# Performance work log

Hardware: AMD Instinct MI355X
Metric: run time of the kernel (lower is better)

The kernel has to match this reference:

```python
import jax, jax.numpy as jnp
import numpy as np

B, S, D = 128, 50, 128
NUM_NODE = 40000
SAMPLE = 12
HOP = 2
ALPHA = 0.2  # leaky-relu slope (opt.alpha)


def _leaky(x, slope=ALPHA):
    return jnp.where(x >= 0, x, slope * x)


def setup_inputs() -> dict:
    key = jax.random.key(0)
    ks = jax.random.split(key, 12)
    stdv = 1.0 / float(np.sqrt(D))
    inputs = jax.random.randint(ks[0], (B, S), 0, NUM_NODE)
    adj = jax.random.randint(ks[1], (B, S, S), 0, 5)
    mask_item = jax.random.randint(ks[2], (B, S), 0, 2).at[:, 0].set(1)
    item = jax.random.randint(ks[3], (B, S), 0, NUM_NODE)
    adj_all = jax.random.randint(ks[4], (NUM_NODE, SAMPLE), 0, NUM_NODE)
    num_weight = jax.random.uniform(ks[5], (NUM_NODE, SAMPLE), dtype=jnp.float32)
    embedding = jax.random.uniform(ks[6], (NUM_NODE, D), minval=-stdv, maxval=stdv, dtype=jnp.float32)
    a_local = jax.random.uniform(ks[7], (4, D), minval=-stdv, maxval=stdv, dtype=jnp.float32)
    agg_w1 = jax.random.uniform(ks[8], (HOP, D + 1, D), minval=-stdv, maxval=stdv, dtype=jnp.float32)
    agg_w2 = jax.random.uniform(ks[9], (HOP, D, 1), minval=-stdv, maxval=stdv, dtype=jnp.float32)
    agg_w3 = jax.random.uniform(ks[10], (HOP, 2 * D, D), minval=-stdv, maxval=stdv, dtype=jnp.float32)
    return dict(inputs=inputs, adj=adj, mask_item=mask_item, item=item,
                adj_all=adj_all, num_weight=num_weight, embedding=embedding,
                a_local=a_local, agg_w1=agg_w1, agg_w2=agg_w2, agg_w3=agg_w3)


def _local_agg(h, adj, a_local):
    # e_k[b,i,j] = leakyrelu(sum_d h[b,i,d]*h[b,j,d]*a_k[d]); never materialize [B,N,N,D]
    e = _leaky(jnp.einsum('bid,bjd,kd->kbij', h, h, a_local))  # [4,B,S,S]
    alpha = jnp.full(e.shape[1:], -9e15, dtype=h.dtype)
    for k in range(4):
        alpha = jnp.where(adj == k + 1, e[k], alpha)
    alpha = jax.nn.softmax(alpha, axis=-1)
    return alpha @ h


def _global_agg(w1, w2, w3, self_v, neigh_v, neigh_w, extra):
    # self_v [B,L,D]; neigh_v [B,L,SAMPLE,D]; neigh_w [B,L,SAMPLE]; extra [B,L,D]
    feat = jnp.concatenate([extra[:, :, None, :] * neigh_v, neigh_w[..., None]], axis=-1)  # [B,L,SAMPLE,D+1]
    a = _leaky(feat @ w1, 0.2)                              # [B,L,SAMPLE,D]
    a = jax.nn.softmax((a @ w2)[..., 0], axis=-1)[..., None]  # [B,L,SAMPLE,1]
    neigh = jnp.sum(a * neigh_v, axis=-2)                   # [B,L,D]
    out = jnp.concatenate([self_v, neigh], axis=-1) @ w3    # [B,L,D]
    return jax.nn.relu(out)


def _forward(inputs, adj, mask_item, item, adj_all, num_weight, embedding,
             a_local, agg_w1, agg_w2, agg_w3):
    h = embedding[inputs]                          # [B,S,D]
    h_local = _local_agg(h, adj, a_local)
    # multi-hop neighbor sampling (index_select into adj_all / num)
    item_neighbors = [inputs]
    weight_neighbors = []
    support = S
    for _ in range(HOP):
        last = item_neighbors[-1].reshape(-1)
        support *= SAMPLE
        item_neighbors.append(adj_all[last].reshape(B, support))
        weight_neighbors.append(num_weight[last].reshape(B, support))
    entity = [embedding[idx] for idx in item_neighbors]
    mask_f = mask_item.astype(h.dtype)
    item_emb = embedding[item] * mask_f[..., None]
    session = (jnp.sum(item_emb, 1) / jnp.sum(mask_f, -1, keepdims=True))[:, None, :]  # [B,1,D]
    for n_hop in range(HOP):
        nxt = []
        for hop in range(HOP - n_hop):
            self_v = entity[hop]
            L = self_v.shape[1]
            neigh_v = entity[hop + 1].reshape(B, L, SAMPLE, D)
            neigh_w = weight_neighbors[hop].reshape(B, L, SAMPLE)
            extra = jnp.broadcast_to(session, (B, L, D))
            nxt.append(_global_agg(agg_w1[n_hop], agg_w2[n_hop], agg_w3[n_hop],
                                   self_v, neigh_v, neigh_w, extra))
        entity = nxt
    h_global = entity[0].reshape(B, S, D)
    # dropout_local / dropout_global are identity in eval mode
    return h_local + h_global


def reference(inputs, adj, mask_item, item, adj_all, num_weight, embedding,
              a_local, agg_w1, agg_w2, agg_w3):
    return _forward(inputs, adj, mask_item, item, adj_all, num_weight, embedding,
                    a_local, agg_w1, agg_w2, agg_w3)
```

## Files before the change

kernel.cpp:

```cpp
#include <hip/hip_runtime.h>
#include <math.h>

#define BATCH 128
#define S 50
#define D 128
#define SAMPLE 12

typedef __attribute__((ext_vector_type(8))) short short8v;
typedef __attribute__((ext_vector_type(4))) float f32x4;
typedef unsigned short u16;

__device__ __forceinline__ float leakyf(float x) { return x >= 0.f ? x : 0.2f * x; }
__device__ __forceinline__ u16 f2bf(float f) {
    union { float f; unsigned u; } v; v.f = f;
    unsigned u = v.u;
    return (u16)((u + 0x7FFFu + ((u >> 16) & 1u)) >> 16);
}
__device__ __forceinline__ float bf2f(u16 h) {
    union { float f; unsigned u; } v; v.u = ((unsigned)h) << 16; return v.f;
}

__global__ __launch_bounds__(256) void setup1_kernel(
    const int* __restrict__ item, const int* __restrict__ mask,
    const int* __restrict__ inputs, const int* __restrict__ adj_all,
    const float* __restrict__ num_weight, const float* __restrict__ emb,
    float* __restrict__ session, int* __restrict__ n1, float* __restrict__ nw0)
{
    const int bx = blockIdx.x, t = threadIdx.x;
    if (bx < BATCH) {
        if (t < 128) {
            float num = 0.f, den = 0.f;
            for (int s = 0; s < S; ++s) {
                float m = (float)mask[bx * S + s];
                num += m * emb[item[bx * S + s] * D + t];
                den += m;
            }
            session[bx * D + t] = num / den;
        }
    } else {
        int idx = (bx - BATCH) * 256 + t;
        if (idx < BATCH * 600) {
            int b = idx / 600, j = idx % 600;
            int node = inputs[b * S + j / SAMPLE];
            n1[idx]  = adj_all[node * SAMPLE + j % SAMPLE];
            nw0[idx] = num_weight[node * SAMPLE + j % SAMPLE];
        }
    }
}

__global__ __launch_bounds__(256) void prep2_kernel(
    const float* __restrict__ emb, const float* __restrict__ w1,
    const float* __restrict__ w3, const float* __restrict__ session,
    const int* __restrict__ adj_all, const float* __restrict__ num_weight,
    const int* __restrict__ n1,
    u16* __restrict__ emb_bf, u16* __restrict__ sw1, u16* __restrict__ w3t,
    int* __restrict__ n2p, int* __restrict__ n1p, float* __restrict__ nw1)
{
    const int bx = blockIdx.x, t = threadIdx.x;
    if (bx < 2500) {
        int idx = bx * 256 + t;
        const float4* src = reinterpret_cast<const float4*>(emb) + (size_t)idx * 2;
        float4 a = src[0], c = src[1];
        u16 o[8] = {f2bf(a.x), f2bf(a.y), f2bf(a.z), f2bf(a.w),
                    f2bf(c.x), f2bf(c.y), f2bf(c.z), f2bf(c.w)};
        *reinterpret_cast<uint4*>(emb_bf + (size_t)idx * 8) = *reinterpret_cast<uint4*>(o);
    } else if (bx < 2756) {
        int id = bx - 2500, hop = id >> 7, b = id & 127;
        const float* w1s = w1 + hop * 129 * 128;
        const float* se = session + b * 128;
        int n = t >> 1, kh = (t & 1) * 64;
        u16* dst = sw1 + (((size_t)(hop * 128 + b) * 128 + n) * 128) + kh;
        for (int kq = 0; kq < 64; kq += 8) {
            u16 o[8];
            #pragma unroll
            for (int e = 0; e < 8; ++e) { int k = kh + kq + e; o[e] = f2bf(w1s[k * 128 + n] * se[k]); }
            *reinterpret_cast<uint4*>(dst + kq) = *reinterpret_cast<uint4*>(o);
        }
    } else if (bx < 2788) {
        int j = (bx - 2756) * 256 + t;
        int hop = j >> 12, r = j & 4095, n = r >> 5, k0 = (r & 31) * 8;
        const float* w3s = w3 + hop * 256 * 128;
        u16 o[8];
        #pragma unroll
        for (int e = 0; e < 8; ++e) o[e] = f2bf(w3s[(k0 + e) * 128 + n]);
        *reinterpret_cast<uint4*>(w3t + ((size_t)hop * 128 + n) * 256 + k0) = *reinterpret_cast<uint4*>(o);
    } else if (bx < 6388) {
        int idx = (bx - 2788) * 256 + t;
        if (idx < BATCH * 7200) {
            int b = idx / 7200, r = idx % 7200;
            int lblk = r / 96, q = r % 96;
            int i = q >> 4, c = q & 15;
            int gm = lblk * 96 + (c >> 2) * 24 + i * 4 + (c & 3);
            int node = n1[b * 600 + gm / SAMPLE];
            int s = gm % SAMPLE;
            n2p[idx] = adj_all[node * SAMPLE + s] << 8;
            nw1[b * 7200 + gm] = num_weight[node * SAMPLE + s];
        }
    } else {
        int idx = (bx - 6388) * 256 + t;
        if (idx < BATCH * 672) {
            int b = idx / 672, r = idx % 672;
            int lblk = r / 96, q = r % 96;
            int i = q >> 4, c = q & 15;
            int gm = lblk * 96 + (c >> 2) * 24 + i * 4 + (c & 3);
            int jc = (gm < 600) ? gm : 0;
            n1p[idx] = n1[b * 600 + jc] << 8;
        }
    }
}

__device__ __forceinline__ int swz(int cg, int kk) { return ((kk & 1) << 2) | cg; }

template <int PATH>
__global__ __launch_bounds__(256, 4) void main_kernel(
    const int* __restrict__ inputs, const int* __restrict__ adj,
    const u16* __restrict__ emb_bf, const float* __restrict__ a_local,
    const int* __restrict__ n1, const int* __restrict__ n2p,
    const int* __restrict__ n1p,
    const float* __restrict__ nw0, const float* __restrict__ nw1,
    const u16* __restrict__ sw1, const float* __restrict__ w1,
    const float* __restrict__ w2, const u16* __restrict__ w3t,
    const u16* __restrict__ in0, const u16* __restrict__ in1,
    u16* __restrict__ o0, u16* __restrict__ o1, float* __restrict__ outf)
{
    __shared__ __align__(16) char smem[35072];
    const int b = blockIdx.y;
    const int t = threadIdx.x;
    const int bx = blockIdx.x;

    if (PATH == 0 && bx == 0) {
        u16*   ht    = (u16*)smem;
        float* alpha = (float*)(smem + 13312);
        u16*   alb   = (u16*)(smem + 23520);

        for (int idx = t; idx < S * D; idx += 256) {
            int i = idx >> 7, d = idx & 127;
            ht[d * 52 + i] = emb_bf[(size_t)inputs[b * S + i] * D + d];
        }
        for (int idx = t; idx < 512; idx += 256) alb[idx] = f2bf(a_local[idx]);
        __syncthreads();

        for (int p = t; p < S * S; p += 256) {
            int i = p / S, j = p % S;
            int a = adj[b * S * S + p];
            float v = -9e15f;
            if (a >= 1 && a <= 4) {
                const u16* ak = alb + (a - 1) * D;
                float dot = 0.f;
                #pragma unroll 4
                for (int d = 0; d < D; ++d)
                    dot += bf2f(ht[d * 52 + i]) * bf2f(ht[d * 52 + j]) * bf2f(ak[d]);
                v = leakyf(dot);
            }
            alpha[i * 51 + j] = v;
        }
        __syncthreads();

        if (t < S) {
            float m = -INFINITY;
            for (int j = 0; j < S; ++j) m = fmaxf(m, alpha[t * 51 + j]);
            float ssum = 0.f;
            for (int j = 0; j < S; ++j) { float e = __expf(alpha[t * 51 + j] - m); alpha[t * 51 + j] = e; ssum += e; }
            float inv = 1.f / ssum;
            for (int j = 0; j < S; ++j) alpha[t * 51 + j] *= inv;
        }
        __syncthreads();

        for (int idx = t; idx < S * D; idx += 256) {
            int i = idx >> 7, d = idx & 127;
            float acc = 0.f;
            #pragma unroll 5
            for (int j = 0; j < S; ++j) acc += alpha[i * 51 + j] * bf2f(ht[d * 52 + j]);
            outf[(size_t)b * S * D + idx] = acc;
        }
        return;
    }

    int mode, lblk, L, Lm, hop;
    const u16 *nsrc, *ssrc;
    const int* ptab; const float* nwTab;
    u16* outb;
    if (PATH == 2)    { mode = 2; lblk = bx;     L = 50;  Lm = 600;  hop = 1; nsrc = in1;    ssrc = in0;    ptab = nullptr;                   nwTab = nw0; outb = nullptr; }
    else if (bx >= 8) { mode = 1; lblk = bx - 8; L = 600; Lm = 7200; hop = 0; nsrc = emb_bf; ssrc = emb_bf; ptab = n2p + (b * 75 + lblk) * 96; nwTab = nw1; outb = o1; }
    else              { mode = 0; lblk = bx - 1; L = 50;  Lm = 600;  hop = 0; nsrc = emb_bf; ssrc = emb_bf; ptab = n1p + (b * 7 + lblk) * 96;  nwTab = nw0; outb = o0; }
    const int l0 = lblk * 8;

    u16*   nvL     = (u16*)smem;
    u16*   A2      = (u16*)(smem + 24576);
    float* score_w = (float*)(smem + 32768);
    float* nwgtL   = (float*)(smem + 34304);
    float* alphL   = (float*)(smem + 34688);

    const u16*   sw1b   = sw1 + (size_t)(hop * 128 + b) * 16384;
    const float* w1last = w1 + hop * 129 * 128 + 128 * 128;
    const float* w2h    = w2 + hop * 128;
    const u16*   w3th   = w3t + hop * 32768;

    const int lane = t & 63, wv = t >> 6, cn = lane & 15, cg = lane >> 4;
    const int nc0 = (2 * wv) * 16 + cn, nc1 = (2 * wv + 1) * 16 + cn;
    const int cS = t & 15;
    const int chunk = t >> 4;

    {
        int kkS = t >> 6, cgS = (t >> 4) & 3;
        int cn2 = cS ^ swz(cgS, kkS);
        #pragma unroll
        for (int i = 0; i < 6; ++i) {
            int off;
            if (PATH == 2) {
                int gm = l0 * 12 + (cn2 >> 2) * 24 + i * 4 + (cn2 & 3);
                if (gm > 599) gm = 599;
                off = (b * 600 + gm) << 8;
            } else {
                off = ptab[i * 16 + cn2];
            }
            uint4 v = *reinterpret_cast<const uint4*>((const char*)nsrc + (unsigned)off + chunk * 16);
            *reinterpret_cast<uint4*>(nvL + (i * 256 + t) * 8) = v;
        }
    }
    {
        uint4 v = make_uint4(0, 0, 0, 0);
        if (cS < 8) {
            int lg = l0 + cS; if (lg >= L) lg = 0;
            int srow;
            if (PATH == 2)      srow = b * 50 + lg;
            else if (mode == 1) srow = n1[b * 600 + lg];
            else                srow = inputs[b * S + lg];
            v = *reinterpret_cast<const uint4*>(ssrc + (size_t)srow * 128 + chunk * 8);
        }
        *reinterpret_cast<uint4*>(A2 + t * 8) = v;
    }
    if (t < 128) {
        int slot = (4 + (t >> 5)) * 64 + ((t >> 3) & 3) * 16 + 8 + (t & 7);
        *reinterpret_cast<uint4*>(A2 + slot * 8) = make_uint4(0, 0, 0, 0);
    }
    if (t < 96) {
        int gm = l0 * 12 + t;
        nwgtL[t] = (gm < Lm) ? nwTab[b * Lm + gm] : 0.f;
    }
    __syncthreads();

    f32x4 acc[6][2];
    #pragma unroll
    for (int mt = 0; mt < 6; ++mt) {
        acc[mt][0] = (f32x4){0.f, 0.f, 0.f, 0.f};
        acc[mt][1] = (f32x4){0.f, 0.f, 0.f, 0.f};
    }
    #pragma unroll
    for (int kk = 0; kk < 4; ++kk) {
        int kb = kk * 32 + cg * 8;
        int lslot = cg * 16 + (cn ^ swz(cg, kk));
        short8v b0 = *reinterpret_cast<const short8v*>(sw1b + nc0 * 128 + kb);
        short8v b1 = *reinterpret_cast<const short8v*>(sw1b + nc1 * 128 + kb);
        #pragma unroll
        for (int mt = 0; mt < 6; ++mt) {
            short8v a = *reinterpret_cast<const short8v*>(nvL + ((mt * 4 + kk) * 64 + lslot) * 8);
            acc[mt][0] = __builtin_amdgcn_mfma_f32_16x16x32_bf16(a, b0, acc[mt][0], 0, 0, 0);
            acc[mt][1] = __builtin_amdgcn_mfma_f32_16x16x32_bf16(a, b1, acc[mt][1], 0, 0, 0);
        }
    }
    {
        float w2v0 = w2h[nc0], w2v1 = w2h[nc1];
        float w1l0 = w1last[nc0], w1l1 = w1last[nc1];
        #pragma unroll
        for (int mt = 0; mt < 6; ++mt) {
            #pragma unroll
            for (int r = 0; r < 4; ++r) {
                int m = cg * 24 + mt * 4 + r;
                float nw = nwgtL[m];
                float v = leakyf(acc[mt][0][r] + nw * w1l0) * w2v0 +
                          leakyf(acc[mt][1][r] + nw * w1l1) * w2v1;
                v += __shfl_xor(v, 1); v += __shfl_xor(v, 2);
                v += __shfl_xor(v, 4); v += __shfl_xor(v, 8);
                if (cn == 0) score_w[m * 4 + wv] = v;
            }
        }
    }
    __syncthreads();

    {
        float alph[24];
        const f32x4* sw4 = reinterpret_cast<const f32x4*>(score_w);
        float mx0 = -1e30f, mx1 = -1e30f;
        #pragma unroll
        for (int q = 0; q < 24; ++q) {
            f32x4 s4 = sw4[cg * 24 + q];
            float s = (s4[0] + s4[1]) + (s4[2] + s4[3]);
            alph[q] = s;
            if (q < 12) mx0 = fmaxf(mx0, s); else mx1 = fmaxf(mx1, s);
        }
        float sm0 = 0.f, sm1 = 0.f;
        #pragma unroll
        for (int q = 0; q < 12; ++q) { alph[q] = __expf(alph[q] - mx0); sm0 += alph[q]; }
        #pragma unroll
        for (int q = 12; q < 24; ++q) { alph[q] = __expf(alph[q] - mx1); sm1 += alph[q]; }
        float i0 = 1.f / sm0, i1 = 1.f / sm1;
        if (cn == 0) {
            #pragma unroll
            for (int q = 0; q < 12; ++q)  alphL[(cg * 2) * 12 + q] = alph[q] * i0;
            #pragma unroll
            for (int q = 12; q < 24; ++q) alphL[(cg * 2 + 1) * 12 + (q - 12)] = alph[q] * i1;
        }
    }

    #pragma unroll 1
    for (int i = 0; i < 4; ++i) {
        int idx = i * 256 + t;
        int l = idx >> 7, d = idx & 127;
        int kkd = d >> 5, cgd = (d >> 3) & 3, el = d & 7;
        int cnb = (l >> 1) * 4;
        int mtb = (l & 1) * 3;
        int fd = swz(cgd, kkd);
        float a = 0.f;
        #pragma unroll
        for (int s = 0; s < 12; ++s) {
            int slot = ((mtb + (s >> 2)) * 4 + kkd) * 64 + cgd * 16 + ((cnb + (s & 3)) ^ fd);
            a += alphL[l * 12 + s] * bf2f(nvL[slot * 8 + el]);
        }
        int slot2 = (4 + kkd) * 64 + cgd * 16 + l;
        A2[slot2 * 8 + el] = f2bf(a);
    }
    __syncthreads();

    #pragma unroll
    for (int j = 0; j < 2; ++j) {
        int nc = (2 * wv + j) * 16 + cn;
        f32x4 acc2 = (f32x4){0.f, 0.f, 0.f, 0.f};
        #pragma unroll
        for (int kk2 = 0; kk2 < 8; ++kk2) {
            short8v a2 = *reinterpret_cast<const short8v*>(A2 + (kk2 * 64 + lane) * 8);
            short8v bb = *reinterpret_cast<const short8v*>(w3th + nc * 256 + kk2 * 32 + cg * 8);
            acc2 = __builtin_amdgcn_mfma_f32_16x16x32_bf16(a2, bb, acc2, 0, 0, 0);
        }
        if (cg < 2) {
            #pragma unroll
            for (int r = 0; r < 4; ++r) {
                int l = cg * 4 + r;
                int lg = l0 + l;
                float v = fmaxf(acc2[r], 0.f);
                if (lg < L) {
                    if (PATH == 2) { float* p = outf + ((size_t)b * 50 + lg) * 128 + nc; *p += v; }
                    else           outb[((size_t)b * L + lg) * 128 + nc] = f2bf(v);
                }
            }
        }
    }
}

extern "C" void kernel_launch(void* const* d_in, const int* in_sizes, int n_in,
                              void* d_out, int out_size, void* d_ws, size_t ws_size,
                              hipStream_t stream)
{
    const int*   inputs     = (const int*)d_in[0];
    const int*   adj        = (const int*)d_in[1];
    const int*   mask_item  = (const int*)d_in[2];
    const int*   item       = (const int*)d_in[3];
    const int*   adj_all    = (const int*)d_in[4];
    const float* num_weight = (const float*)d_in[5];
    const float* embedding  = (const float*)d_in[6];
    const float* a_local    = (const float*)d_in[7];
    const float* agg_w1     = (const float*)d_in[8];
    const float* agg_w2     = (const float*)d_in[9];
    const float* agg_w3     = (const float*)d_in[10];
    float* out = (float*)d_out;

    char* w = (char*)d_ws;
    float* ws_session = (float*)(w);
    int*   ws_n1      = (int*)(w + 65536);
    float* ws_nw0     = (float*)(w + 372736);
    float* ws_nw1     = (float*)(w + 679936);
    int*   ws_n2p     = (int*)(w + 4366336);
    int*   ws_n1p     = (int*)(w + 8052736);
    u16*   ws_emb     = (u16*)(w + 8396800);
    u16*   ws_sw1     = (u16*)(w + 18636800);
    u16*   ws_w3t     = (u16*)(w + 27025408);
    u16*   ws_out0    = (u16*)(w + 27156480);
    u16*   ws_out1    = (u16*)(w + 28794880);

    setup1_kernel<<<dim3(BATCH + 300), 256, 0, stream>>>(
        item, mask_item, inputs, adj_all, num_weight, embedding,
        ws_session, ws_n1, ws_nw0);
    prep2_kernel<<<dim3(6724), 256, 0, stream>>>(
        embedding, agg_w1, agg_w3, ws_session, adj_all, num_weight, ws_n1,
        ws_emb, ws_sw1, ws_w3t, ws_n2p, ws_n1p, ws_nw1);

    main_kernel<0><<<dim3(83, BATCH), 256, 0, stream>>>(
        inputs, adj, ws_emb, a_local, ws_n1, ws_n2p, ws_n1p, ws_nw0, ws_nw1,
        ws_sw1, agg_w1, agg_w2, ws_w3t,
        nullptr, nullptr, ws_out0, ws_out1, out);

    main_kernel<2><<<dim3(7, BATCH), 256, 0, stream>>>(
        inputs, adj, ws_emb, a_local, ws_n1, ws_n2p, ws_n1p, ws_nw0, ws_nw1,
        ws_sw1, agg_w1, agg_w2, ws_w3t,
        ws_out0, ws_out1, nullptr, nullptr, out);
}
```

Baseline: 356.6 us.

## Assign one wave per neighbor row with register-resident A fragments

```diff
diff --git a/kernel.cpp b/kernel.cpp
--- a/kernel.cpp
+++ b/kernel.cpp
@@ -54,7 +54,7 @@
     const int* __restrict__ adj_all, const float* __restrict__ num_weight,
     const int* __restrict__ n1,
     u16* __restrict__ emb_bf, u16* __restrict__ sw1, u16* __restrict__ w3t,
-    int* __restrict__ n2p, int* __restrict__ n1p, float* __restrict__ nw1)
+    int* __restrict__ n2o, float* __restrict__ nw1)
 {
     const int bx = blockIdx.x, t = threadIdx.x;
     if (bx < 2500) {
@@ -84,46 +84,30 @@
         #pragma unroll
         for (int e = 0; e < 8; ++e) o[e] = f2bf(w3s[(k0 + e) * 128 + n]);
         *reinterpret_cast<uint4*>(w3t + ((size_t)hop * 128 + n) * 256 + k0) = *reinterpret_cast<uint4*>(o);
-    } else if (bx < 6388) {
+    } else {
         int idx = (bx - 2788) * 256 + t;
         if (idx < BATCH * 7200) {
-            int b = idx / 7200, r = idx % 7200;
-            int lblk = r / 96, q = r % 96;
-            int i = q >> 4, c = q & 15;
-            int gm = lblk * 96 + (c >> 2) * 24 + i * 4 + (c & 3);
-            int node = n1[b * 600 + gm / SAMPLE];
-            int s = gm % SAMPLE;
-            n2p[idx] = adj_all[node * SAMPLE + s] << 8;
-            nw1[b * 7200 + gm] = num_weight[node * SAMPLE + s];
-        }
-    } else {
-        int idx = (bx - 6388) * 256 + t;
-        if (idx < BATCH * 672) {
-            int b = idx / 672, r = idx % 672;
-            int lblk = r / 96, q = r % 96;
-            int i = q >> 4, c = q & 15;
-            int gm = lblk * 96 + (c >> 2) * 24 + i * 4 + (c & 3);
-            int jc = (gm < 600) ? gm : 0;
-            n1p[idx] = n1[b * 600 + jc] << 8;
-        }
-    }
-}
-
-__device__ __forceinline__ int swz(int cg, int kk) { return ((kk & 1) << 2) | cg; }
+            int b = idx / 7200, j = idx % 7200;
+            int node = n1[b * 600 + j / SAMPLE];
+            int s = j % SAMPLE;
+            n2o[idx] = adj_all[node * SAMPLE + s] << 8;
+            nw1[idx] = num_weight[node * SAMPLE + s];
+        }
+    }
+}
 
 template <int PATH>
-__global__ __launch_bounds__(256, 4) void main_kernel(
+__global__ __launch_bounds__(512, 4) void main_kernel(
     const int* __restrict__ inputs, const int* __restrict__ adj,
     const u16* __restrict__ emb_bf, const float* __restrict__ a_local,
-    const int* __restrict__ n1, const int* __restrict__ n2p,
-    const int* __restrict__ n1p,
+    const int* __restrict__ n1, const int* __restrict__ n2o,
     const float* __restrict__ nw0, const float* __restrict__ nw1,
     const u16* __restrict__ sw1, const float* __restrict__ w1,
     const float* __restrict__ w2, const u16* __restrict__ w3t,
     const u16* __restrict__ in0, const u16* __restrict__ in1,
     u16* __restrict__ o0, u16* __restrict__ o1, float* __restrict__ outf)
 {
-    __shared__ __align__(16) char smem[35072];
+    __shared__ __align__(16) char smem[41472];
     const int b = blockIdx.y;
     const int t = threadIdx.x;
     const int bx = blockIdx.x;
@@ -133,14 +117,15 @@
         float* alpha = (float*)(smem + 13312);
         u16*   alb   = (u16*)(smem + 23520);
 
-        for (int idx = t; idx < S * D; idx += 256) {
+        for (int idx = t; idx < S * D; idx += 512) {
             int i = idx >> 7, d = idx & 127;
             ht[d * 52 + i] = emb_bf[(size_t)inputs[b * S + i] * D + d];
         }
-        for (int idx = t; idx < 512; idx += 256) alb[idx] = f2bf(a_local[idx]);
+        if (t < 512) { if (t < 512 && t < 512) {} }
+        for (int idx = t; idx < 512; idx += 512) alb[idx] = f2bf(a_local[idx]);
         __syncthreads();
 
-        for (int p = t; p < S * S; p += 256) {
+        for (int p = t; p < S * S; p += 512) {
             int i = p / S, j = p % S;
             int a = adj[b * S * S + p];
             float v = -9e15f;
@@ -166,7 +151,7 @@
         }
         __syncthreads();
 
-        for (int idx = t; idx < S * D; idx += 256) {
+        for (int idx = t; idx < S * D; idx += 512) {
             int i = idx >> 7, d = idx & 127;
             float acc = 0.f;
             #pragma unroll 5
@@ -176,156 +161,128 @@
         return;
     }
 
-    int mode, lblk, L, Lm, hop;
+    int mode, lblk, L, hop, nstr;
     const u16 *nsrc, *ssrc;
-    const int* ptab; const float* nwTab;
+    const float* nwTab;
     u16* outb;
-    if (PATH == 2)    { mode = 2; lblk = bx;     L = 50;  Lm = 600;  hop = 1; nsrc = in1;    ssrc = in0;    ptab = nullptr;                   nwTab = nw0; outb = nullptr; }
-    else if (bx >= 8) { mode = 1; lblk = bx - 8; L = 600; Lm = 7200; hop = 0; nsrc = emb_bf; ssrc = emb_bf; ptab = n2p + (b * 75 + lblk) * 96; nwTab = nw1; outb = o1; }
-    else              { mode = 0; lblk = bx - 1; L = 50;  Lm = 600;  hop = 0; nsrc = emb_bf; ssrc = emb_bf; ptab = n1p + (b * 7 + lblk) * 96;  nwTab = nw0; outb = o0; }
+    if (PATH == 2)    { mode = 2; lblk = bx;     L = 50;  hop = 1; nstr = 600;  nsrc = in1;    ssrc = in0;    nwTab = nw0; outb = nullptr; }
+    else if (bx >= 8) { mode = 1; lblk = bx - 8; L = 600; hop = 0; nstr = 7200; nsrc = emb_bf; ssrc = emb_bf; nwTab = nw1; outb = o1; }
+    else              { mode = 0; lblk = bx - 1; L = 50;  hop = 0; nstr = 600;  nsrc = emb_bf; ssrc = emb_bf; nwTab = nw0; outb = o0; }
     const int l0 = lblk * 8;
 
-    u16*   nvL     = (u16*)smem;
-    u16*   A2      = (u16*)(smem + 24576);
-    float* score_w = (float*)(smem + 32768);
-    float* nwgtL   = (float*)(smem + 34304);
-    float* alphL   = (float*)(smem + 34688);
+    const int wv = t >> 6, lane = t & 63, cn = lane & 15, cg = lane >> 4;
+    const int l = l0 + wv;
+    const int lc = (l < L) ? l : (L - 1);
+
+    u16*   nvw   = (u16*)(smem) + wv * 2048;
+    u16*   A2    = (u16*)(smem + 32768);
+    float* alphL = (float*)(smem + 40960);
 
     const u16*   sw1b   = sw1 + (size_t)(hop * 128 + b) * 16384;
     const float* w1last = w1 + hop * 129 * 128 + 128 * 128;
     const float* w2h    = w2 + hop * 128;
     const u16*   w3th   = w3t + hop * 32768;
 
-    const int lane = t & 63, wv = t >> 6, cn = lane & 15, cg = lane >> 4;
-    const int nc0 = (2 * wv) * 16 + cn, nc1 = (2 * wv + 1) * 16 + cn;
-    const int cS = t & 15;
-    const int chunk = t >> 4;
-
+    int sidx = (cn < 12) ? cn : 11;
+    unsigned off;
+    if (mode == 1)      off = (unsigned)n2o[b * 7200 + lc * 12 + sidx];
+    else if (mode == 0) off = (unsigned)n1[b * 600 + lc * 12 + sidx] << 8;
+    else                off = (unsigned)(b * 600 + lc * 12 + sidx) << 8;
+
+    short8v aF[4];
+    #pragma unroll
+    for (int kk = 0; kk < 4; ++kk)
+        aF[kk] = *reinterpret_cast<const short8v*>((const char*)nsrc + off + (kk * 32 + cg * 8) * 2);
+    #pragma unroll
+    for (int kk = 0; kk < 4; ++kk)
+        *reinterpret_cast<short8v*>((char*)nvw + cn * 256 + ((kk * 64 + cg * 16) ^ ((cn & 7) << 4))) = aF[kk];
+
+    float nwr[4];
+    #pragma unroll
+    for (int r = 0; r < 4; ++r) {
+        int row = cg * 4 + r; int rr = (row < 12) ? row : 11;
+        nwr[r] = nwTab[b * nstr + lc * 12 + rr];
+    }
+
+    if (lane < 16) {
+        int kk = lane >> 2, cg2 = lane & 3;
+        int lg = l; if (lg >= L) lg = 0;
+        int srow;
+        if (PATH == 2)      srow = b * 50 + lg;
+        else if (mode == 1) srow = n1[b * 600 + lg];
+        else                srow = inputs[b * S + lg];
+        uint4 v = *reinterpret_cast<const uint4*>(ssrc + (size_t)srow * 128 + kk * 32 + cg2 * 8);
+        *reinterpret_cast<uint4*>(A2 + (kk * 64 + cg2 * 16 + wv) * 8) = v;
+    } else if (lane < 48) {
+        int idx = wv * 32 + (lane - 16);
+        int slot = (idx >> 5) * 64 + ((idx >> 3) & 3) * 16 + 8 + (idx & 7);
+        *reinterpret_cast<uint4*>(A2 + slot * 8) = make_uint4(0, 0, 0, 0);
+    }
+
+    f32x4 acc[8];
+    #pragma unroll
+    for (int nt = 0; nt < 8; ++nt) acc[nt] = (f32x4){0.f, 0.f, 0.f, 0.f};
+    #pragma unroll
+    for (int kk = 0; kk < 4; ++kk) {
+        #pragma unroll
+        for (int nt = 0; nt < 8; ++nt) {
+            short8v bF = *reinterpret_cast<const short8v*>(sw1b + (nt * 16 + cn) * 128 + kk * 32 + cg * 8);
+            acc[nt] = __builtin_amdgcn_mfma_f32_16x16x32_bf16(aF[kk], bF, acc[nt], 0, 0, 0);
+        }
+    }
+
+    float sc[4];
+    #pragma unroll
+    for (int r = 0; r < 4; ++r) {
+        float v = 0.f;
+        #pragma unroll
+        for (int nt = 0; nt < 8; ++nt) {
+            int ncol = nt * 16 + cn;
+            v += leakyf(acc[nt][r] + nwr[r] * w1last[ncol]) * w2h[ncol];
+        }
+        v += __shfl_xor(v, 1); v += __shfl_xor(v, 2);
+        v += __shfl_xor(v, 4); v += __shfl_xor(v, 8);
+        sc[r] = v;
+    }
     {
-        int kkS = t >> 6, cgS = (t >> 4) & 3;
-        int cn2 = cS ^ swz(cgS, kkS);
-        #pragma unroll
-        for (int i = 0; i < 6; ++i) {
-            int off;
-            if (PATH == 2) {
-                int gm = l0 * 12 + (cn2 >> 2) * 24 + i * 4 + (cn2 & 3);
-                if (gm > 599) gm = 599;
-                off = (b * 600 + gm) << 8;
-            } else {
-                off = ptab[i * 16 + cn2];
-            }
-            uint4 v = *reinterpret_cast<const uint4*>((const char*)nsrc + (unsigned)off + chunk * 16);
-            *reinterpret_cast<uint4*>(nvL + (i * 256 + t) * 8) = v;
-        }
-    }
-    {
-        uint4 v = make_uint4(0, 0, 0, 0);
-        if (cS < 8) {
-            int lg = l0 + cS; if (lg >= L) lg = 0;
-            int srow;
-            if (PATH == 2)      srow = b * 50 + lg;
-            else if (mode == 1) srow = n1[b * 600 + lg];
-            else                srow = inputs[b * S + lg];
-            v = *reinterpret_cast<const uint4*>(ssrc + (size_t)srow * 128 + chunk * 8);
-        }
-        *reinterpret_cast<uint4*>(A2 + t * 8) = v;
-    }
-    if (t < 128) {
-        int slot = (4 + (t >> 5)) * 64 + ((t >> 3) & 3) * 16 + 8 + (t & 7);
-        *reinterpret_cast<uint4*>(A2 + slot * 8) = make_uint4(0, 0, 0, 0);
-    }
-    if (t < 96) {
-        int gm = l0 * 12 + t;
-        nwgtL[t] = (gm < Lm) ? nwTab[b * Lm + gm] : 0.f;
-    }
-    __syncthreads();
-
-    f32x4 acc[6][2];
-    #pragma unroll
-    for (int mt = 0; mt < 6; ++mt) {
-        acc[mt][0] = (f32x4){0.f, 0.f, 0.f, 0.f};
-        acc[mt][1] = (f32x4){0.f, 0.f, 0.f, 0.f};
-    }
-    #pragma unroll
-    for (int kk = 0; kk < 4; ++kk) {
-        int kb = kk * 32 + cg * 8;
-        int lslot = cg * 16 + (cn ^ swz(cg, kk));
-        short8v b0 = *reinterpret_cast<const short8v*>(sw1b + nc0 * 128 + kb);
-        short8v b1 = *reinterpret_cast<const short8v*>(sw1b + nc1 * 128 + kb);
-        #pragma unroll
-        for (int mt = 0; mt < 6; ++mt) {
-            short8v a = *reinterpret_cast<const short8v*>(nvL + ((mt * 4 + kk) * 64 + lslot) * 8);
-            acc[mt][0] = __builtin_amdgcn_mfma_f32_16x16x32_bf16(a, b0, acc[mt][0], 0, 0, 0);
-            acc[mt][1] = __builtin_amdgcn_mfma_f32_16x16x32_bf16(a, b1, acc[mt][1], 0, 0, 0);
-        }
-    }
-    {
-        float w2v0 = w2h[nc0], w2v1 = w2h[nc1];
-        float w1l0 = w1last[nc0], w1l1 = w1last[nc1];
-        #pragma unroll
-        for (int mt = 0; mt < 6; ++mt) {
-            #pragma unroll
-            for (int r = 0; r < 4; ++r) {
-                int m = cg * 24 + mt * 4 + r;
-                float nw = nwgtL[m];
-                float v = leakyf(acc[mt][0][r] + nw * w1l0) * w2v0 +
-                          leakyf(acc[mt][1][r] + nw * w1l1) * w2v1;
-                v += __shfl_xor(v, 1); v += __shfl_xor(v, 2);
-                v += __shfl_xor(v, 4); v += __shfl_xor(v, 8);
-                if (cn == 0) score_w[m * 4 + wv] = v;
-            }
-        }
-    }
-    __syncthreads();
-
-    {
-        float alph[24];
-        const f32x4* sw4 = reinterpret_cast<const f32x4*>(score_w);
-        float mx0 = -1e30f, mx1 = -1e30f;
-        #pragma unroll
-        for (int q = 0; q < 24; ++q) {
-            f32x4 s4 = sw4[cg * 24 + q];
-            float s = (s4[0] + s4[1]) + (s4[2] + s4[3]);
-            alph[q] = s;
-            if (q < 12) mx0 = fmaxf(mx0, s); else mx1 = fmaxf(mx1, s);
-        }
-        float sm0 = 0.f, sm1 = 0.f;
-        #pragma unroll
-        for (int q = 0; q < 12; ++q) { alph[q] = __expf(alph[q] - mx0); sm0 += alph[q]; }
-        #pragma unroll
-        for (int q = 12; q < 24; ++q) { alph[q] = __expf(alph[q] - mx1); sm1 += alph[q]; }
-        float i0 = 1.f / sm0, i1 = 1.f / sm1;
+        float mx = -1e30f;
+        #pragma unroll
+        for (int r = 0; r < 4; ++r) if (cg * 4 + r < 12) mx = fmaxf(mx, sc[r]);
+        mx = fmaxf(mx, __shfl_xor(mx, 16)); mx = fmaxf(mx, __shfl_xor(mx, 32));
+        float e[4]; float sm = 0.f;
+        #pragma unroll
+        for (int r = 0; r < 4; ++r) {
+            e[r] = (cg * 4 + r < 12) ? __expf(sc[r] - mx) : 0.f;
+            sm += e[r];
+        }
+        sm += __shfl_xor(sm, 16); sm += __shfl_xor(sm, 32);
+        float inv = 1.f / sm;
         if (cn == 0) {
             #pragma unroll
-            for (int q = 0; q < 12; ++q)  alphL[(cg * 2) * 12 + q] = alph[q] * i0;
-            #pragma unroll
-            for (int q = 12; q < 24; ++q) alphL[(cg * 2 + 1) * 12 + (q - 12)] = alph[q] * i1;
-        }
-    }
-
-    #pragma unroll 1
-    for (int i = 0; i < 4; ++i) {
-        int idx = i * 256 + t;
-        int l = idx >> 7, d = idx & 127;
-        int kkd = d >> 5, cgd = (d >> 3) & 3, el = d & 7;
-        int cnb = (l >> 1) * 4;
-        int mtb = (l & 1) * 3;
-        int fd = swz(cgd, kkd);
-        float a = 0.f;
-        #pragma unroll
-        for (int s = 0; s < 12; ++s) {
-            int slot = ((mtb + (s >> 2)) * 4 + kkd) * 64 + cgd * 16 + ((cnb + (s & 3)) ^ fd);
-            a += alphL[l * 12 + s] * bf2f(nvL[slot * 8 + el]);
-        }
-        int slot2 = (4 + kkd) * 64 + cgd * 16 + l;
-        A2[slot2 * 8 + el] = f2bf(a);
+            for (int r = 0; r < 4; ++r)
+                if (cg * 4 + r < 12) alphL[wv * 16 + cg * 4 + r] = e[r] * inv;
+        }
+    }
+
+    {
+        float a0 = 0.f, a1 = 0.f;
+        #pragma unroll
+        for (int s2 = 0; s2 < 12; ++s2) {
+            unsigned pk = *reinterpret_cast<const unsigned*>(
+                (const char*)nvw + s2 * 256 + ((lane * 4) ^ ((s2 & 7) << 4)));
+            float al = alphL[wv * 16 + s2];
+            a0 += al * bf2f((u16)(pk & 0xffff));
+            a1 += al * bf2f((u16)(pk >> 16));
+        }
+        unsigned pk2 = ((unsigned)f2bf(a1) << 16) | f2bf(a0);
+        int slot = (4 + cg) * 64 + ((lane >> 2) & 3) * 16 + wv;
+        *reinterpret_cast<unsigned*>((char*)A2 + slot * 16 + (lane & 3) * 4) = pk2;
     }
     __syncthreads();
 
-    #pragma unroll
-    for (int j = 0; j < 2; ++j) {
-        int nc = (2 * wv + j) * 16 + cn;
+    {
         f32x4 acc2 = (f32x4){0.f, 0.f, 0.f, 0.f};
+        int nc = wv * 16 + cn;
         #pragma unroll
         for (int kk2 = 0; kk2 < 8; ++kk2) {
             short8v a2 = *reinterpret_cast<const short8v*>(A2 + (kk2 * 64 + lane) * 8);
@@ -335,8 +292,8 @@
         if (cg < 2) {
             #pragma unroll
             for (int r = 0; r < 4; ++r) {
-                int l = cg * 4 + r;
-                int lg = l0 + l;
+                int row = cg * 4 + r;
+                int lg = l0 + row;
                 float v = fmaxf(acc2[r], 0.f);
                 if (lg < L) {
                     if (PATH == 2) { float* p = outf + ((size_t)b * 50 + lg) * 128 + nc; *p += v; }
@@ -369,28 +326,27 @@
     int*   ws_n1      = (int*)(w + 65536);
     float* ws_nw0     = (float*)(w + 372736);
     float* ws_nw1     = (float*)(w + 679936);
-    int*   ws_n2p     = (int*)(w + 4366336);
-    int*   ws_n1p     = (int*)(w + 8052736);
-    u16*   ws_emb     = (u16*)(w + 8396800);
-    u16*   ws_sw1     = (u16*)(w + 18636800);
-    u16*   ws_w3t     = (u16*)(w + 27025408);
-    u16*   ws_out0    = (u16*)(w + 27156480);
-    u16*   ws_out1    = (u16*)(w + 28794880);
+    int*   ws_n2o     = (int*)(w + 4366336);
+    u16*   ws_emb     = (u16*)(w + 8052736);
+    u16*   ws_sw1     = (u16*)(w + 18292736);
+    u16*   ws_w3t     = (u16*)(w + 26681344);
+    u16*   ws_out0    = (u16*)(w + 26812416);
+    u16*   ws_out1    = (u16*)(w + 28450816);
 
     setup1_kernel<<<dim3(BATCH + 300), 256, 0, stream>>>(
         item, mask_item, inputs, adj_all, num_weight, embedding,
         ws_session, ws_n1, ws_nw0);
-    prep2_kernel<<<dim3(6724), 256, 0, stream>>>(
+    prep2_kernel<<<dim3(6388), 256, 0, stream>>>(
         embedding, agg_w1, agg_w3, ws_session, adj_all, num_weight, ws_n1,
-        ws_emb, ws_sw1, ws_w3t, ws_n2p, ws_n1p, ws_nw1);
-
-    main_kernel<0><<<dim3(83, BATCH), 256, 0, stream>>>(
-        inputs, adj, ws_emb, a_local, ws_n1, ws_n2p, ws_n1p, ws_nw0, ws_nw1,
+        ws_emb, ws_sw1, ws_w3t, ws_n2o, ws_nw1);
+
+    main_kernel<0><<<dim3(83, BATCH), 512, 0, stream>>>(
+        inputs, adj, ws_emb, a_local, ws_n1, ws_n2o, ws_nw0, ws_nw1,
         ws_sw1, agg_w1, agg_w2, ws_w3t,
         nullptr, nullptr, ws_out0, ws_out1, out);
 
-    main_kernel<2><<<dim3(7, BATCH), 256, 0, stream>>>(
-        inputs, adj, ws_emb, a_local, ws_n1, ws_n2p, ws_n1p, ws_nw0, ws_nw1,
+    main_kernel<2><<<dim3(7, BATCH), 512, 0, stream>>>(
+        inputs, adj, ws_emb, a_local, ws_n1, ws_n2o, ws_nw0, ws_nw1,
         ws_sw1, agg_w1, agg_w2, ws_w3t,
         ws_out0, ws_out1, nullptr, nullptr, out);
 }
```

Measured after the change: 574.6 us. +61.1%, slower.

## Convert main kernel to persistent per-batch blocks with double-buffered async LDS loads

Applied to the files above, without the earlier changes.

```diff
diff --git a/kernel.cpp b/kernel.cpp
--- a/kernel.cpp
+++ b/kernel.cpp
@@ -18,6 +18,15 @@
 }
 __device__ __forceinline__ float bf2f(u16 h) {
     union { float f; unsigned u; } v; v.u = ((unsigned)h) << 16; return v.f;
+}
+__device__ __forceinline__ void gld_lds16(const void* g, void* l) {
+    __builtin_amdgcn_global_load_lds(
+        (const __attribute__((address_space(1))) void*)g,
+        (__attribute__((address_space(3))) void*)l, 16, 0, 0);
+}
+__device__ __forceinline__ void barrier_lds_only() {
+    asm volatile("s_waitcnt lgkmcnt(0)" ::: "memory");
+    __builtin_amdgcn_s_barrier();
 }
 
 __global__ __launch_bounds__(256) void setup1_kernel(
@@ -52,9 +61,10 @@
     const float* __restrict__ emb, const float* __restrict__ w1,
     const float* __restrict__ w3, const float* __restrict__ session,
     const int* __restrict__ adj_all, const float* __restrict__ num_weight,
-    const int* __restrict__ n1,
+    const int* __restrict__ n1, const int* __restrict__ inputs,
     u16* __restrict__ emb_bf, u16* __restrict__ sw1, u16* __restrict__ w3t,
-    int* __restrict__ n2p, int* __restrict__ n1p, float* __restrict__ nw1)
+    int* __restrict__ n2p, int* __restrict__ n1p, float* __restrict__ nw1,
+    int* __restrict__ sfo)
 {
     const int bx = blockIdx.x, t = threadIdx.x;
     if (bx < 2500) {
@@ -96,7 +106,7 @@
             n2p[idx] = adj_all[node * SAMPLE + s] << 8;
             nw1[b * 7200 + gm] = num_weight[node * SAMPLE + s];
         }
-    } else {
+    } else if (bx < 6724) {
         int idx = (bx - 6388) * 256 + t;
         if (idx < BATCH * 672) {
             int b = idx / 672, r = idx % 672;
@@ -106,29 +116,259 @@
             int jc = (gm < 600) ? gm : 0;
             n1p[idx] = n1[b * 600 + jc] << 8;
         }
-    }
-}
-
-__device__ __forceinline__ int swz(int cg, int kk) { return ((kk & 1) << 2) | cg; }
+    } else {
+        int idx = (bx - 6724) * 256 + t;
+        if (idx < BATCH * 82 * 16) {
+            int b = idx / (82 * 16), r2 = idx % (82 * 16), u = r2 >> 4, r = r2 & 15;
+            int sov;
+            if (u < 75) {
+                int l = u * 8 + (r & 7);
+                sov = n1[b * 600 + l] << 8;
+            } else {
+                int l = (u - 75) * 8 + (r & 7); if (l >= 50) l = 0;
+                sov = inputs[b * S + l] << 8;
+            }
+            sfo[idx] = sov;
+        }
+    }
+}
 
 template <int PATH>
-__global__ __launch_bounds__(256, 4) void main_kernel(
+__device__ __forceinline__ void ldregs(int u, int b, int t, int cidx, int task0,
+    const int* __restrict__ n2p, const int* __restrict__ n1p,
+    const float* __restrict__ nw0, const float* __restrict__ nw1,
+    unsigned po[6], float& nwr)
+{
+    if (PATH == 0) {
+        const int* pt; const float* nws;
+        if (u < 75) { pt = n2p + (b * 75 + u) * 96; nws = nw1 + (size_t)b * 7200 + (size_t)u * 96; }
+        else        { pt = n1p + (b * 7 + (u - 75)) * 96; nws = nw0 + (size_t)b * 600 + (size_t)(u - 75) * 96; }
+        #pragma unroll
+        for (int i = 0; i < 6; ++i) po[i] = (unsigned)pt[i * 16 + cidx];
+        nwr = (t < 96) ? nws[t] : 0.f;
+    } else {
+        int l0_ = task0 * 8;
+        #pragma unroll
+        for (int i = 0; i < 6; ++i) {
+            int gm = l0_ * 12 + (cidx >> 2) * 24 + i * 4 + (cidx & 3);
+            if (gm > 599) gm = 599;
+            po[i] = (unsigned)((b * 600 + gm) << 8);
+        }
+        int mm = l0_ * 12 + t; if (mm > 599) mm = 599;
+        nwr = (t < 96) ? nw0[(size_t)b * 600 + mm] : 0.f;
+    }
+}
+
+template <int PATH>
+__device__ __forceinline__ unsigned ldsoff(int u, int b, int cS, int task0,
+                                           const int* __restrict__ sfo)
+{
+    if (PATH == 0) return (unsigned)sfo[(b * 82 + u) * 16 + cS];
+    int lg = task0 * 8 + (cS & 7); if (lg >= 50) lg = 0;
+    return (unsigned)((b * 50 + lg) << 8);
+}
+
+template <int PATH>
+__global__ __launch_bounds__(256, 2) void persist_kernel(
     const int* __restrict__ inputs, const int* __restrict__ adj,
     const u16* __restrict__ emb_bf, const float* __restrict__ a_local,
-    const int* __restrict__ n1, const int* __restrict__ n2p,
-    const int* __restrict__ n1p,
+    const int* __restrict__ n2p, const int* __restrict__ n1p,
+    const int* __restrict__ sfo,
     const float* __restrict__ nw0, const float* __restrict__ nw1,
     const u16* __restrict__ sw1, const float* __restrict__ w1,
     const float* __restrict__ w2, const u16* __restrict__ w3t,
     const u16* __restrict__ in0, const u16* __restrict__ in1,
     u16* __restrict__ o0, u16* __restrict__ o1, float* __restrict__ outf)
 {
-    __shared__ __align__(16) char smem[35072];
+    __shared__ __align__(16) char smem[60032];
     const int b = blockIdx.y;
+    const int s = blockIdx.x;
     const int t = threadIdx.x;
-    const int bx = blockIdx.x;
-
-    if (PATH == 0 && bx == 0) {
+
+    int task0, ntask;
+    if (PATH == 0) {
+        const int st0[5] = {0, 20, 41, 62, 82};
+        task0 = st0[s]; ntask = st0[s + 1] - task0;
+    } else { task0 = s; ntask = 1; }
+    const int taskL = task0 + ntask - 1;
+
+    u16* nvLb0     = (u16*)smem;
+    u16* nvLb1     = (u16*)(smem + 24576);
+    u16* A2        = (u16*)(smem + 49152);
+    float* score_w = (float*)(smem + 57344);
+    float* nwgt    = (float*)(smem + 58880);
+    float* alphL   = (float*)(smem + 59648);
+
+    const int hop = (PATH == 2) ? 1 : 0;
+    const u16*   sw1b   = sw1 + (size_t)(hop * 128 + b) * 16384;
+    const float* w1last = w1 + hop * 129 * 128 + 128 * 128;
+    const float* w2h    = w2 + hop * 128;
+    const u16*   w3th   = w3t + hop * 32768;
+    const u16*   nsrc   = (PATH == 2) ? in1 : emb_bf;
+    const u16*   ssrc   = (PATH == 2) ? in0 : emb_bf;
+
+    const int lane = t & 63, wv = t >> 6, cn = lane & 15, cg = lane >> 4;
+    const int nc0 = (2 * wv) * 16 + cn, nc1 = (2 * wv + 1) * 16 + cn;
+    const int cS = t & 15, chunk = t >> 4;
+    const int cidx = cS ^ ((((t >> 6) & 1) << 2) | ((t >> 4) & 3));
+
+    short8v B1a[4], B1b[4];
+    #pragma unroll
+    for (int kk = 0; kk < 4; ++kk) {
+        B1a[kk] = *reinterpret_cast<const short8v*>(sw1b + nc0 * 128 + kk * 32 + cg * 8);
+        B1b[kk] = *reinterpret_cast<const short8v*>(sw1b + nc1 * 128 + kk * 32 + cg * 8);
+    }
+    const float w2v0 = w2h[nc0], w2v1 = w2h[nc1];
+    const float w1l0 = w1last[nc0], w1l1 = w1last[nc1];
+
+    unsigned po[6]; float nwr; unsigned soff; uint4 sdat;
+    ldregs<PATH>(task0, b, t, cidx, task0, n2p, n1p, nw0, nw1, po, nwr);
+    soff = ldsoff<PATH>(task0, b, cS, task0, sfo);
+    {
+        char* db = (char*)nvLb0 + wv * 1024;
+        #pragma unroll
+        for (int i = 0; i < 6; ++i)
+            gld_lds16((const char*)nsrc + po[i] + chunk * 16, db + i * 4096);
+    }
+    if (t < 96) nwgt[t] = nwr;
+    sdat = *reinterpret_cast<const uint4*>((const char*)ssrc + soff + chunk * 16);
+    {
+        int un = (task0 + 1 < taskL) ? task0 + 1 : taskL;
+        ldregs<PATH>(un, b, t, cidx, task0, n2p, n1p, nw0, nw1, po, nwr);
+        soff = ldsoff<PATH>(un, b, cS, task0, sfo);
+    }
+    __syncthreads();
+
+    for (int i = 0; i < ntask; ++i) {
+        const int cur = i & 1;
+        u16* nvL = cur ? nvLb1 : nvLb0;
+
+        *reinterpret_cast<uint4*>(A2 + t * 8) = sdat;
+
+        if (i + 1 < ntask) {
+            char* db = (char*)(cur ? nvLb0 : nvLb1) + wv * 1024;
+            #pragma unroll
+            for (int q = 0; q < 6; ++q)
+                gld_lds16((const char*)nsrc + po[q] + chunk * 16, db + q * 4096);
+            if (t < 96) nwgt[(cur ^ 1) * 96 + t] = nwr;
+        }
+        sdat = *reinterpret_cast<const uint4*>((const char*)ssrc + soff + chunk * 16);
+        {
+            int u2 = (task0 + i + 2 < taskL) ? task0 + i + 2 : taskL;
+            ldregs<PATH>(u2, b, t, cidx, task0, n2p, n1p, nw0, nw1, po, nwr);
+            soff = ldsoff<PATH>(u2, b, cS, task0, sfo);
+        }
+
+        f32x4 acc[6][2];
+        #pragma unroll
+        for (int mt = 0; mt < 6; ++mt) {
+            acc[mt][0] = (f32x4){0.f, 0.f, 0.f, 0.f};
+            acc[mt][1] = (f32x4){0.f, 0.f, 0.f, 0.f};
+        }
+        #pragma unroll
+        for (int kk = 0; kk < 4; ++kk) {
+            int lslot = cg * 16 + (cn ^ (((kk & 1) << 2) | cg));
+            #pragma unroll
+            for (int mt = 0; mt < 6; ++mt) {
+                short8v a = *reinterpret_cast<const short8v*>(nvL + ((mt * 4 + kk) * 64 + lslot) * 8);
+                acc[mt][0] = __builtin_amdgcn_mfma_f32_16x16x32_bf16(a, B1a[kk], acc[mt][0], 0, 0, 0);
+                acc[mt][1] = __builtin_amdgcn_mfma_f32_16x16x32_bf16(a, B1b[kk], acc[mt][1], 0, 0, 0);
+            }
+        }
+        {
+            const float* nwg = nwgt + cur * 96;
+            #pragma unroll
+            for (int mt = 0; mt < 6; ++mt) {
+                #pragma unroll
+                for (int r = 0; r < 4; ++r) {
+                    int m = cg * 24 + mt * 4 + r;
+                    float nw = nwg[m];
+                    float v = leakyf(acc[mt][0][r] + nw * w1l0) * w2v0 +
+                              leakyf(acc[mt][1][r] + nw * w1l1) * w2v1;
+                    v += __shfl_xor(v, 1); v += __shfl_xor(v, 2);
+                    v += __shfl_xor(v, 4); v += __shfl_xor(v, 8);
+                    if (cn == 0) score_w[m * 4 + wv] = v;
+                }
+            }
+        }
+        barrier_lds_only();
+
+        {
+            float alph[24];
+            const f32x4* sw4 = reinterpret_cast<const f32x4*>(score_w);
+            float mx0 = -1e30f, mx1 = -1e30f;
+            #pragma unroll
+            for (int q = 0; q < 24; ++q) {
+                f32x4 s4 = sw4[cg * 24 + q];
+                float sv = (s4[0] + s4[1]) + (s4[2] + s4[3]);
+                alph[q] = sv;
+                if (q < 12) mx0 = fmaxf(mx0, sv); else mx1 = fmaxf(mx1, sv);
+            }
+            float sm0 = 0.f, sm1 = 0.f;
+            #pragma unroll
+            for (int q = 0; q < 12; ++q)  { alph[q] = __expf(alph[q] - mx0); sm0 += alph[q]; }
+            #pragma unroll
+            for (int q = 12; q < 24; ++q) { alph[q] = __expf(alph[q] - mx1); sm1 += alph[q]; }
+            float i0 = 1.f / sm0, i1 = 1.f / sm1;
+            if (cn == 0) {
+                #pragma unroll
+                for (int q = 0; q < 12; ++q)  alphL[(cg * 2) * 12 + q] = alph[q] * i0;
+                #pragma unroll
+                for (int q = 12; q < 24; ++q) alphL[(cg * 2 + 1) * 12 + (q - 12)] = alph[q] * i1;
+            }
+        }
+        #pragma unroll 1
+        for (int ii = 0; ii < 4; ++ii) {
+            int idx = ii * 256 + t;
+            int l = idx >> 7, d = idx & 127;
+            int kkd = d >> 5, cgd = (d >> 3) & 3, el = d & 7;
+            int cnb = (l >> 1) * 4, mtb = (l & 1) * 3;
+            int fd = ((kkd & 1) << 2) | cgd;
+            float a = 0.f;
+            #pragma unroll
+            for (int s2 = 0; s2 < 12; ++s2) {
+                int slot = ((mtb + (s2 >> 2)) * 4 + kkd) * 64 + cgd * 16 + ((cnb + (s2 & 3)) ^ fd);
+                a += alphL[l * 12 + s2] * bf2f(nvL[slot * 8 + el]);
+            }
+            A2[((4 + kkd) * 64 + cgd * 16 + l) * 8 + el] = f2bf(a);
+        }
+        barrier_lds_only();
+
+        {
+            int uu = task0 + i;
+            u16* outp = nullptr; int l0c, Lc;
+            if (PATH == 0) {
+                if (uu < 75) { outp = o1; l0c = uu * 8; Lc = 600; }
+                else         { outp = o0; l0c = (uu - 75) * 8; Lc = 50; }
+            } else { l0c = task0 * 8; Lc = 50; }
+
+            #pragma unroll
+            for (int j = 0; j < 2; ++j) {
+                int nc = (2 * wv + j) * 16 + cn;
+                f32x4 acc2 = (f32x4){0.f, 0.f, 0.f, 0.f};
+                #pragma unroll
+                for (int kk2 = 0; kk2 < 8; ++kk2) {
+                    short8v a2 = *reinterpret_cast<const short8v*>(A2 + (kk2 * 64 + lane) * 8);
+                    short8v bb = *reinterpret_cast<const short8v*>(w3th + nc * 256 + kk2 * 32 + cg * 8);
+                    acc2 = __builtin_amdgcn_mfma_f32_16x16x32_bf16(a2, bb, acc2, 0, 0, 0);
+                }
+                if (cg < 2) {
+                    #pragma unroll
+                    for (int r = 0; r < 4; ++r) {
+                        int lg = l0c + cg * 4 + r;
+                        float v = fmaxf(acc2[r], 0.f);
+                        if (lg < Lc) {
+                            if (PATH == 2) { float* p = outf + ((size_t)b * 50 + lg) * 128 + nc; *p += v; }
+                            else           outp[((size_t)b * Lc + lg) * 128 + nc] = f2bf(v);
+                        }
+                    }
+                }
+            }
+        }
+        __syncthreads();
+    }
+
+    if (PATH == 0 && s == 0) {
         u16*   ht    = (u16*)smem;
         float* alpha = (float*)(smem + 13312);
         u16*   alb   = (u16*)(smem + 23520);
@@ -172,177 +412,6 @@
             #pragma unroll 5
             for (int j = 0; j < S; ++j) acc += alpha[i * 51 + j] * bf2f(ht[d * 52 + j]);
             outf[(size_t)b * S * D + idx] = acc;
-        }
-        return;
-    }
-
-    int mode, lblk, L, Lm, hop;
-    const u16 *nsrc, *ssrc;
-    const int* ptab; const float* nwTab;
-    u16* outb;
-    if (PATH == 2)    { mode = 2; lblk = bx;     L = 50;  Lm = 600;  hop = 1; nsrc = in1;    ssrc = in0;    ptab = nullptr;                   nwTab = nw0; outb = nullptr; }
-    else if (bx >= 8) { mode = 1; lblk = bx - 8; L = 600; Lm = 7200; hop = 0; nsrc = emb_bf; ssrc = emb_bf; ptab = n2p + (b * 75 + lblk) * 96; nwTab = nw1; outb = o1; }
-    else              { mode = 0; lblk = bx - 1; L = 50;  Lm = 600;  hop = 0; nsrc = emb_bf; ssrc = emb_bf; ptab = n1p + (b * 7 + lblk) * 96;  nwTab = nw0; outb = o0; }
-    const int l0 = lblk * 8;
-
-    u16*   nvL     = (u16*)smem;
-    u16*   A2      = (u16*)(smem + 24576);
-    float* score_w = (float*)(smem + 32768);
-    float* nwgtL   = (float*)(smem + 34304);
-    float* alphL   = (float*)(smem + 34688);
-
-    const u16*   sw1b   = sw1 + (size_t)(hop * 128 + b) * 16384;
-    const float* w1last = w1 + hop * 129 * 128 + 128 * 128;
-    const float* w2h    = w2 + hop * 128;
-    const u16*   w3th   = w3t + hop * 32768;
-
-    const int lane = t & 63, wv = t >> 6, cn = lane & 15, cg = lane >> 4;
-    const int nc0 = (2 * wv) * 16 + cn, nc1 = (2 * wv + 1) * 16 + cn;
-    const int cS = t & 15;
-    const int chunk = t >> 4;
-
-    {
-        int kkS = t >> 6, cgS = (t >> 4) & 3;
-        int cn2 = cS ^ swz(cgS, kkS);
-        #pragma unroll
-        for (int i = 0; i < 6; ++i) {
-            int off;
-            if (PATH == 2) {
-                int gm = l0 * 12 + (cn2 >> 2) * 24 + i * 4 + (cn2 & 3);
-                if (gm > 599) gm = 599;
-                off = (b * 600 + gm) << 8;
-            } else {
-                off = ptab[i * 16 + cn2];
-            }
-            uint4 v = *reinterpret_cast<const uint4*>((const char*)nsrc + (unsigned)off + chunk * 16);
-            *reinterpret_cast<uint4*>(nvL + (i * 256 + t) * 8) = v;
-        }
-    }
-    {
-        uint4 v = make_uint4(0, 0, 0, 0);
-        if (cS < 8) {
-            int lg = l0 + cS; if (lg >= L) lg = 0;
-            int srow;
-            if (PATH == 2)      srow = b * 50 + lg;
-            else if (mode == 1) srow = n1[b * 600 + lg];
-            else                srow = inputs[b * S + lg];
-            v = *reinterpret_cast<const uint4*>(ssrc + (size_t)srow * 128 + chunk * 8);
-        }
-        *reinterpret_cast<uint4*>(A2 + t * 8) = v;
-    }
-    if (t < 128) {
-        int slot = (4 + (t >> 5)) * 64 + ((t >> 3) & 3) * 16 + 8 + (t & 7);
-        *reinterpret_cast<uint4*>(A2 + slot * 8) = make_uint4(0, 0, 0, 0);
-    }
-    if (t < 96) {
-        int gm = l0 * 12 + t;
-        nwgtL[t] = (gm < Lm) ? nwTab[b * Lm + gm] : 0.f;
-    }
-    __syncthreads();
-
-    f32x4 acc[6][2];
-    #pragma unroll
-    for (int mt = 0; mt < 6; ++mt) {
-        acc[mt][0] = (f32x4){0.f, 0.f, 0.f, 0.f};
-        acc[mt][1] = (f32x4){0.f, 0.f, 0.f, 0.f};
-    }
-    #pragma unroll
-    for (int kk = 0; kk < 4; ++kk) {
-        int kb = kk * 32 + cg * 8;
-        int lslot = cg * 16 + (cn ^ swz(cg, kk));
-        short8v b0 = *reinterpret_cast<const short8v*>(sw1b + nc0 * 128 + kb);
-        short8v b1 = *reinterpret_cast<const short8v*>(sw1b + nc1 * 128 + kb);
-        #pragma unroll
-        for (int mt = 0; mt < 6; ++mt) {
-            short8v a = *reinterpret_cast<const short8v*>(nvL + ((mt * 4 + kk) * 64 + lslot) * 8);
-            acc[mt][0] = __builtin_amdgcn_mfma_f32_16x16x32_bf16(a, b0, acc[mt][0], 0, 0, 0);
-            acc[mt][1] = __builtin_amdgcn_mfma_f32_16x16x32_bf16(a, b1, acc[mt][1], 0, 0, 0);
-        }
-    }
-    {
-        float w2v0 = w2h[nc0], w2v1 = w2h[nc1];
-        float w1l0 = w1last[nc0], w1l1 = w1last[nc1];
-        #pragma unroll
-        for (int mt = 0; mt < 6; ++mt) {
-            #pragma unroll
-            for (int r = 0; r < 4; ++r) {
-                int m = cg * 24 + mt * 4 + r;
-                float nw = nwgtL[m];
-                float v = leakyf(acc[mt][0][r] + nw * w1l0) * w2v0 +
-                          leakyf(acc[mt][1][r] + nw * w1l1) * w2v1;
-                v += __shfl_xor(v, 1); v += __shfl_xor(v, 2);
-                v += __shfl_xor(v, 4); v += __shfl_xor(v, 8);
-                if (cn == 0) score_w[m * 4 + wv] = v;
-            }
-        }
-    }
-    __syncthreads();
-
-    {
-        float alph[24];
-        const f32x4* sw4 = reinterpret_cast<const f32x4*>(score_w);
-        float mx0 = -1e30f, mx1 = -1e30f;
-        #pragma unroll
-        for (int q = 0; q < 24; ++q) {
-            f32x4 s4 = sw4[cg * 24 + q];
-            float s = (s4[0] + s4[1]) + (s4[2] + s4[3]);
-            alph[q] = s;
-            if (q < 12) mx0 = fmaxf(mx0, s); else mx1 = fmaxf(mx1, s);
-        }
-        float sm0 = 0.f, sm1 = 0.f;
-        #pragma unroll
-        for (int q = 0; q < 12; ++q) { alph[q] = __expf(alph[q] - mx0); sm0 += alph[q]; }
-        #pragma unroll
-        for (int q = 12; q < 24; ++q) { alph[q] = __expf(alph[q] - mx1); sm1 += alph[q]; }
-        float i0 = 1.f / sm0, i1 = 1.f / sm1;
-        if (cn == 0) {
-            #pragma unroll
-            for (int q = 0; q < 12; ++q)  alphL[(cg * 2) * 12 + q] = alph[q] * i0;
-            #pragma unroll
-            for (int q = 12; q < 24; ++q) alphL[(cg * 2 + 1) * 12 + (q - 12)] = alph[q] * i1;
-        }
-    }
-
-    #pragma unroll 1
-    for (int i = 0; i < 4; ++i) {
-        int idx = i * 256 + t;
-        int l = idx >> 7, d = idx & 127;
-        int kkd = d >> 5, cgd = (d >> 3) & 3, el = d & 7;
-        int cnb = (l >> 1) * 4;
-        int mtb = (l & 1) * 3;
-        int fd = swz(cgd, kkd);
-        float a = 0.f;
-        #pragma unroll
-        for (int s = 0; s < 12; ++s) {
-            int slot = ((mtb + (s >> 2)) * 4 + kkd) * 64 + cgd * 16 + ((cnb + (s & 3)) ^ fd);
-            a += alphL[l * 12 + s] * bf2f(nvL[slot * 8 + el]);
-        }
-        int slot2 = (4 + kkd) * 64 + cgd * 16 + l;
-        A2[slot2 * 8 + el] = f2bf(a);
-    }
-    __syncthreads();
-
-    #pragma unroll
-    for (int j = 0; j < 2; ++j) {
-        int nc = (2 * wv + j) * 16 + cn;
-        f32x4 acc2 = (f32x4){0.f, 0.f, 0.f, 0.f};
-        #pragma unroll
-        for (int kk2 = 0; kk2 < 8; ++kk2) {
-            short8v a2 = *reinterpret_cast<const short8v*>(A2 + (kk2 * 64 + lane) * 8);
-            short8v bb = *reinterpret_cast<const short8v*>(w3th + nc * 256 + kk2 * 32 + cg * 8);
-            acc2 = __builtin_amdgcn_mfma_f32_16x16x32_bf16(a2, bb, acc2, 0, 0, 0);
-        }
-        if (cg < 2) {
-            #pragma unroll
-            for (int r = 0; r < 4; ++r) {
-                int l = cg * 4 + r;
-                int lg = l0 + l;
-                float v = fmaxf(acc2[r], 0.f);
-                if (lg < L) {
-                    if (PATH == 2) { float* p = outf + ((size_t)b * 50 + lg) * 128 + nc; *p += v; }
-                    else           outb[((size_t)b * L + lg) * 128 + nc] = f2bf(v);
-                }
-            }
         }
     }
 }
@@ -371,26 +440,27 @@
     float* ws_nw1     = (float*)(w + 679936);
     int*   ws_n2p     = (int*)(w + 4366336);
     int*   ws_n1p     = (int*)(w + 8052736);
-    u16*   ws_emb     = (u16*)(w + 8396800);
-    u16*   ws_sw1     = (u16*)(w + 18636800);
-    u16*   ws_w3t     = (u16*)(w + 27025408);
-    u16*   ws_out0    = (u16*)(w + 27156480);
-    u16*   ws_out1    = (u16*)(w + 28794880);
+    int*   ws_sfo     = (int*)(w + 8396800);
+    u16*   ws_emb     = (u16*)(w + 9068544);
+    u16*   ws_sw1     = (u16*)(w + 19308544);
+    u16*   ws_w3t     = (u16*)(w + 27697152);
+    u16*   ws_out0    = (u16*)(w + 27828224);
+    u16*   ws_out1    = (u16*)(w + 29466624);
 
     setup1_kernel<<<dim3(BATCH + 300), 256, 0, stream>>>(
         item, mask_item, inputs, adj_all, num_weight, embedding,
         ws_session, ws_n1, ws_nw0);
-    prep2_kernel<<<dim3(6724), 256, 0, stream>>>(
+    prep2_kernel<<<dim3(7380), 256, 0, stream>>>(
         embedding, agg_w1, agg_w3, ws_session, adj_all, num_weight, ws_n1,
-        ws_emb, ws_sw1, ws_w3t, ws_n2p, ws_n1p, ws_nw1);
-
-    main_kernel<0><<<dim3(83, BATCH), 256, 0, stream>>>(
-        inputs, adj, ws_emb, a_local, ws_n1, ws_n2p, ws_n1p, ws_nw0, ws_nw1,
+        inputs, ws_emb, ws_sw1, ws_w3t, ws_n2p, ws_n1p, ws_nw1, ws_sfo);
+
+    persist_kernel<0><<<dim3(4, BATCH), 256, 0, stream>>>(
+        inputs, adj, ws_emb, a_local, ws_n2p, ws_n1p, ws_sfo, ws_nw0, ws_nw1,
         ws_sw1, agg_w1, agg_w2, ws_w3t,
         nullptr, nullptr, ws_out0, ws_out1, out);
 
-    main_kernel<2><<<dim3(7, BATCH), 256, 0, stream>>>(
-        inputs, adj, ws_emb, a_local, ws_n1, ws_n2p, ws_n1p, ws_nw0, ws_nw1,
+    persist_kernel<2><<<dim3(7, BATCH), 256, 0, stream>>>(
+        inputs, adj, ws_emb, a_local, ws_n2p, ws_n1p, ws_sfo, ws_nw0, ws_nw1,
         ws_sw1, agg_w1, agg_w2, ws_w3t,
         ws_out0, ws_out1, nullptr, nullptr, out);
 }
```

New measurement: 403.1 us. +13.0%, slower.
